# Kernel tuning notes

Measured on AMD Instinct MI355X. Metric: run time of the kernel, lower is better.

## Reference

```python
import jax, jax.numpy as jnp
import numpy as np

B, N, C_IN, C_OUT = 8, 4096, 64, 64
NEG_INF = -9e15
LEAKY_SLOPE = 0.01  # torch F.leaky_relu default


def setup_inputs() -> dict:
    key = jax.random.key(0)
    kx, ka, kw, kq, kk = jax.random.split(key, 5)
    X = jax.random.normal(kx, (B, N, C_IN), dtype=jnp.float32)
    A = jax.random.randint(ka, (N, N), 0, 2, dtype=jnp.int32)
    # xavier_uniform with gain=1.414 ~ scaled uniform; plain scaled normal is fine for a numeric reference
    def xavier(k, shape):
        fan_in, fan_out = shape
        bound = 1.414 * np.sqrt(6.0 / (fan_in + fan_out))
        return jax.random.uniform(k, shape, jnp.float32, -bound, bound)
    weight = xavier(kw, (C_IN, C_OUT))
    query = xavier(kq, (C_IN, C_OUT))
    key_p = xavier(kk, (C_IN, C_OUT))
    return {"X": X, "A": A, "weight": weight, "query": query, "key_p": key_p}


def reference(X, A, weight, query, key_p):
    n = X.shape[1]
    idx = jnp.arange(n)
    adj = A.at[idx, idx].set(1)  # add self-loops
    out = jnp.einsum('bni,io->bno', X, weight)
    q = jnp.einsum('bni,io->bno', X, query)
    k = jnp.einsum('bni,io->bno', X, key_p)
    att = jnp.einsum('bnd,bmd->bnm', q, k)          # QK^T, (B,N,N)
    att = jax.nn.leaky_relu(att, LEAKY_SLOPE)
    att = jnp.where(adj[None, :, :] > 0, att, NEG_INF)
    att = jax.nn.softmax(att, axis=-1)
    # dropout p=0 and/or eval mode -> identity
    return jnp.einsum('bnm,bmo->bno', att, out)
```

## Files before the change

kernel.cpp:

```cpp
#include <hip/hip_runtime.h>
#include <stdint.h>

#define BATCH 8
#define NN 4096
#define CC 64
#define MASKV -1.0e30f
#define LOG2E 1.4426950408889634f

typedef _Float16 half8 __attribute__((ext_vector_type(8)));
typedef __fp16 fp16x2 __attribute__((ext_vector_type(2)));
typedef float f32x4 __attribute__((ext_vector_type(4)));
typedef float f32x16 __attribute__((ext_vector_type(16)));

__device__ __forceinline__ unsigned pk_rtz(float a, float b) {
    union { fp16x2 h; unsigned u; } r;
    r.h = __builtin_amdgcn_cvt_pkrtz(a, b);
    return r.u;
}

__global__ __launch_bounds__(256) void gat_proj(
    const float* __restrict__ X, const float* __restrict__ W0,
    const float* __restrict__ Wq, const float* __restrict__ Wk,
    _Float16* __restrict__ qh,
    _Float16* __restrict__ kb, _Float16* __restrict__ vt)
{
    __shared__ alignas(16) _Float16 WTh[3][64][72];
    __shared__ alignas(16) _Float16 WTl[3][64][72];
    const int t = threadIdx.x;
    const float* Ws[3] = {W0, Wq, Wk};
    for (int e = t; e < 4096; e += 256) {
        int k = e >> 6, c = e & 63;
        #pragma unroll
        for (int m = 0; m < 3; ++m) {
            float w = Ws[m][e];
            _Float16 hi = (_Float16)w;
            WTh[m][c][k] = hi;
            WTl[m][c][k] = (_Float16)(w - (float)hi);
        }
    }
    __syncthreads();
    const int lane = t & 63, wv = t >> 6;
    const int cl = lane & 15, g = lane >> 4;
    {
        int tile = blockIdx.x * 4 + wv;
        int gr = tile * 16;
        const float* xr = X + (size_t)(gr + cl) * CC;
        half8 xh[2], xl[2];
        #pragma unroll
        for (int kf = 0; kf < 2; ++kf) {
            f32x4 a0 = *(const f32x4*)(xr + g*8 + kf*32);
            f32x4 a1 = *(const f32x4*)(xr + g*8 + kf*32 + 4);
            half8 h, l;
            #pragma unroll
            for (int j = 0; j < 4; ++j) {
                _Float16 h0 = (_Float16)a0[j], h1 = (_Float16)a1[j];
                h[j]   = h0; l[j]   = (_Float16)(a0[j] - (float)h0);
                h[j+4] = h1; l[j+4] = (_Float16)(a1[j] - (float)h1);
            }
            xh[kf] = h; xl[kf] = l;
        }
        #pragma unroll
        for (int mat = 1; mat <= 2; ++mat) {
            #pragma unroll
            for (int nt = 0; nt < 4; ++nt) {
                f32x4 acc = {0.f, 0.f, 0.f, 0.f};
                #pragma unroll
                for (int kf = 0; kf < 2; ++kf) {
                    half8 bh = *(const half8*)&WTh[mat][nt*16 + cl][g*8 + kf*32];
                    half8 bl = *(const half8*)&WTl[mat][nt*16 + cl][g*8 + kf*32];
                    acc = __builtin_amdgcn_mfma_f32_16x16x32_f16(xh[kf], bh, acc, 0, 0, 0);
                    acc = __builtin_amdgcn_mfma_f32_16x16x32_f16(xl[kf], bh, acc, 0, 0, 0);
                    acc = __builtin_amdgcn_mfma_f32_16x16x32_f16(xh[kf], bl, acc, 0, 0, 0);
                }
                #pragma unroll
                for (int i = 0; i < 4; ++i) {
                    size_t off = (size_t)(gr + 4*g + i) * CC + nt*16 + cl;
                    if (mat == 1) qh[off] = (_Float16)(acc[i] * LOG2E);
                    else          kb[off] = (_Float16)acc[i];
                }
            }
        }
        {
            int b = gr >> 12, n0 = gr & (NN - 1);
            #pragma unroll
            for (int mt = 0; mt < 4; ++mt) {
                f32x4 acc = {0.f, 0.f, 0.f, 0.f};
                #pragma unroll
                for (int kf = 0; kf < 2; ++kf) {
                    half8 ah = *(const half8*)&WTh[0][mt*16 + cl][g*8 + kf*32];
                    half8 al = *(const half8*)&WTl[0][mt*16 + cl][g*8 + kf*32];
                    acc = __builtin_amdgcn_mfma_f32_16x16x32_f16(ah, xh[kf], acc, 0, 0, 0);
                    acc = __builtin_amdgcn_mfma_f32_16x16x32_f16(al, xh[kf], acc, 0, 0, 0);
                    acc = __builtin_amdgcn_mfma_f32_16x16x32_f16(ah, xl[kf], acc, 0, 0, 0);
                }
                #pragma unroll
                for (int i = 0; i < 4; ++i) {
                    int co = mt*16 + 4*g + i;
                    vt[((size_t)b * CC + co) * NN + n0 + cl] = (_Float16)acc[i];
                }
            }
        }
    }
}

__global__ __launch_bounds__(256) void gat_mask(const int* __restrict__ A,
                                                unsigned short* __restrict__ M16)
{
    const int row = blockIdx.x;
    const int w16 = threadIdx.x;
    const int4* ap = (const int4*)(A + (size_t)row * NN + w16 * 16);
    unsigned m = 0;
    #pragma unroll
    for (int j = 0; j < 4; ++j) {
        int4 a = ap[j];
        m |= (a.x != 0 ? 1u : 0u) << (4*j);
        m |= (a.y != 0 ? 1u : 0u) << (4*j + 1);
        m |= (a.z != 0 ? 1u : 0u) << (4*j + 2);
        m |= (a.w != 0 ? 1u : 0u) << (4*j + 3);
    }
    if (w16 == (row >> 4)) m |= 1u << (row & 15);
    M16[(size_t)row * 256 + w16] = (unsigned short)m;
}

__global__ __launch_bounds__(256) void gat_attn(
    const _Float16* __restrict__ qg,
    const _Float16* __restrict__ kf16, const _Float16* __restrict__ vtb,
    const unsigned long long* __restrict__ M,
    _Float16* __restrict__ po, float2* __restrict__ pml)
{
    __shared__ alignas(16) _Float16 Kt[2][64][64];
    __shared__ alignas(16) _Float16 Vt[2][64][64];
    __shared__ alignas(8) uint2 LUT[16];
    const int t = threadIdx.x;
    const int lane = t & 63, wv = t >> 6;
    const int q32 = lane & 31, hi = lane >> 5;
    const int blk = blockIdx.x;
    const int b  = blk & 7;
    const int sp = (blk >> 3) & 3;
    const int qb = blk >> 5;
    const int Q0 = qb * 128 + wv * 32;
    const int c0 = sp * 16;
    const int swz = (q32 & 7) << 4;

    if (t < 16) {
        unsigned n = t;
        LUT[n] = make_uint2(((n & 1u) ? 0x0000FFFFu : 0u) | ((n & 2u) ? 0xFFFF0000u : 0u),
                            ((n & 4u) ? 0x0000FFFFu : 0u) | ((n & 8u) ? 0xFFFF0000u : 0u));
    }

    const int soff = (((t >> 3) * 128 + (t & 7) * 16) ^ (((t >> 3) & 7) << 4));

    half8 qf[4];
    {
        const _Float16* qr = qg + ((size_t)b * NN + Q0 + q32) * CC + hi * 8;
        #pragma unroll
        for (int kf = 0; kf < 4; ++kf) qf[kf] = *(const half8*)(qr + kf * 16);
    }
    const _Float16* kg = kf16 + (size_t)b * NN * CC;
    const _Float16* vg = vtb + (size_t)b * CC * NN;

    f32x16 o0 = {}, o1 = {};
    float m_run = 0.f, l_run = 0.f;

    uint4 pk0, pk1, pv0, pv1;
    unsigned long long pm;
    auto loadchunk = [&](int kcg) {
        const uint4* ks = (const uint4*)(kg + (size_t)kcg * 64 * CC);
        pk0 = ks[t];
        pk1 = ks[t + 256];
        const _Float16* vs = vg + kcg * 64;
        pv0 = *(const uint4*)(vs + (size_t)(t >> 3) * NN + (t & 7) * 8);
        pv1 = *(const uint4*)(vs + (size_t)((t >> 3) + 32) * NN + (t & 7) * 8);
        pm  = M[(size_t)(Q0 + q32) * 64 + kcg];
    };
    auto stash = [&](int bufi) {
        char* kd = (char*)&Kt[bufi][0][0];
        char* vd = (char*)&Vt[bufi][0][0];
        *(uint4*)(kd + soff) = pk0;
        *(uint4*)(kd + soff + 4096) = pk1;
        *(uint4*)(vd + soff) = pv0;
        *(uint4*)(vd + soff + 4096) = pv1;
    };
    auto pkmax = [](unsigned a, unsigned b) {
        unsigned d;
        asm("v_pk_max_f16 %0, %1, %2" : "=v"(d) : "v"(a), "v"(b));
        return d;
    };

    loadchunk(c0);
    unsigned long long cm = pm;
    stash(0);
    __syncthreads();

    for (int kc = 0; kc < 16; ++kc) {
        const int cur = kc & 1;
        if (kc < 15) loadchunk(c0 + kc + 1);

        const char* kbase = (const char*)&Kt[cur][0][0] + q32 * 128;
        __builtin_amdgcn_s_setprio(1);
        f32x16 s0 = {}, s1 = {};
        #pragma unroll
        for (int kf = 0; kf < 4; ++kf) {
            const int col = (kf * 32 + hi * 16) ^ swz;
            half8 ka0 = *(const half8*)(kbase + col);
            half8 ka1 = *(const half8*)(kbase + 4096 + col);
            s0 = __builtin_amdgcn_mfma_f32_32x32x16_f16(ka0, qf[kf], s0, 0, 0, 0);
            s1 = __builtin_amdgcn_mfma_f32_32x32x16_f16(ka1, qf[kf], s1, 0, 0, 0);
        }
        __builtin_amdgcn_s_setprio(0);

        const unsigned wlo = (unsigned)cm, whi = (unsigned)(cm >> 32);
        unsigned hm[16];
        #pragma unroll
        for (int kt = 0; kt < 2; ++kt) {
            unsigned w = kt ? whi : wlo;
            #pragma unroll
            for (int a = 0; a < 4; ++a) {
                unsigned nib = (w >> (8 * a + 4 * hi)) & 15u;
                uint2 e = LUT[nib];
                hm[kt*8 + 2*a]     = e.x;
                hm[kt*8 + 2*a + 1] = e.y;
            }
        }
        {
            unsigned sm[16];
            #pragma unroll
            for (int j = 0; j < 8; ++j) {
                sm[j]   = pk_rtz(s0[2*j], s0[2*j+1]) & hm[j];
                sm[8+j] = pk_rtz(s1[2*j], s1[2*j+1]) & hm[8+j];
            }
            unsigned u0 = pkmax(pkmax(pkmax(sm[0],sm[1]),  pkmax(sm[2],sm[3])),
                                pkmax(pkmax(sm[4],sm[5]),  pkmax(sm[6],sm[7])));
            unsigned u1 = pkmax(pkmax(pkmax(sm[8],sm[9]),  pkmax(sm[10],sm[11])),
                                pkmax(pkmax(sm[12],sm[13]),pkmax(sm[14],sm[15])));
            union { unsigned u; fp16x2 h; } tu; tu.u = pkmax(u0, u1);
            float mx = fmaxf(fmaxf((float)tu.h[0], (float)tu.h[1]), 0.f);
            mx = fmaxf(mx, __shfl_xor(mx, 32));
            if (__any(mx > m_run)) {
                float nm = fmaxf(m_run, mx);
                float alpha = __builtin_amdgcn_exp2f(m_run - nm);
                m_run = nm;
                l_run *= alpha;
                #pragma unroll
                for (int i = 0; i < 16; ++i) { o0[i] *= alpha; o1[i] *= alpha; }
            }
        }
        unsigned wp[16];
        #pragma unroll
        for (int j = 0; j < 8; ++j) {
            float p0 = __builtin_amdgcn_exp2f(fmaxf(s0[2*j]   - m_run, fmaf(0.01f, s0[2*j],   -m_run)));
            float p1 = __builtin_amdgcn_exp2f(fmaxf(s0[2*j+1] - m_run, fmaf(0.01f, s0[2*j+1], -m_run)));
            float p2 = __builtin_amdgcn_exp2f(fmaxf(s1[2*j]   - m_run, fmaf(0.01f, s1[2*j],   -m_run)));
            float p3 = __builtin_amdgcn_exp2f(fmaxf(s1[2*j+1] - m_run, fmaf(0.01f, s1[2*j+1], -m_run)));
            wp[j]   = pk_rtz(p0, p1) & hm[j];
            wp[8+j] = pk_rtz(p2, p3) & hm[8+j];
        }
        {
            union { unsigned u; fp16x2 h; } z; z.u = 0u;
            fp16x2 acc = z.h;
            #pragma unroll
            for (int j4 = 0; j4 < 4; ++j4) {
                union { unsigned u; fp16x2 h; } x0, x1, x2, x3;
                x0.u = wp[4*j4]; x1.u = wp[4*j4+1]; x2.u = wp[4*j4+2]; x3.u = wp[4*j4+3];
                acc += (x0.h + x1.h) + (x2.h + x3.h);
            }
            l_run += (float)acc[0] + (float)acc[1];
        }
        if (kc < 15) stash(cur ^ 1);
        #pragma unroll
        for (int g4 = 0; g4 < 4; ++g4) {
            unsigned w0 = wp[4*g4+0], w1 = wp[4*g4+1];
            unsigned w2 = wp[4*g4+2], w3 = wp[4*g4+3];
            unsigned u = hi ? w0 : w2;
            unsigned v = hi ? w1 : w3;
            unsigned su = (unsigned)__shfl_xor((int)u, 32);
            unsigned sv = (unsigned)__shfl_xor((int)v, 32);
            wp[4*g4+0] = hi ? su : w0;
            wp[4*g4+1] = hi ? sv : w1;
            wp[4*g4+2] = hi ? w2 : su;
            wp[4*g4+3] = hi ? w3 : sv;
        }
        const char* vb = (const char*)&Vt[cur][0][0] + q32 * 128;
        __builtin_amdgcn_s_setprio(1);
        #pragma unroll
        for (int kc4 = 0; kc4 < 4; ++kc4) {
            union { unsigned u[4]; half8 h; } pb;
            pb.u[0] = wp[4*kc4+0]; pb.u[1] = wp[4*kc4+1];
            pb.u[2] = wp[4*kc4+2]; pb.u[3] = wp[4*kc4+3];
            const int col = (kc4 * 32 + hi * 16) ^ swz;
            half8 vf0 = *(const half8*)(vb + col);
            half8 vf1 = *(const half8*)(vb + 4096 + col);
            o0 = __builtin_amdgcn_mfma_f32_32x32x16_f16(vf0, pb.h, o0, 0, 0, 0);
            o1 = __builtin_amdgcn_mfma_f32_32x32x16_f16(vf1, pb.h, o1, 0, 0, 0);
        }
        __builtin_amdgcn_s_setprio(0);
        cm = pm;
        if (kc < 15) __syncthreads();
    }

    float lt = l_run + __shfl_xor(l_run, 32);
    size_t base = (size_t)sp * (BATCH * NN) + (size_t)b * NN + Q0 + q32;
    _Float16* orow = po + base * 64;
    #pragma unroll
    for (int a = 0; a < 4; ++a) {
        {
            uint2 ow = { pk_rtz(o0[4*a], o0[4*a+1]), pk_rtz(o0[4*a+2], o0[4*a+3]) };
            *(uint2*)(orow + 8*a + 4*hi) = ow;
        }
        {
            uint2 ow = { pk_rtz(o1[4*a], o1[4*a+1]), pk_rtz(o1[4*a+2], o1[4*a+3]) };
            *(uint2*)(orow + 32 + 8*a + 4*hi) = ow;
        }
    }
    if (hi == 0) pml[base] = make_float2(m_run, lt);
}

__global__ __launch_bounds__(256) void gat_comb(
    const _Float16* __restrict__ po, const float2* __restrict__ pml,
    float* __restrict__ out)
{
    int gid = blockIdx.x * 256 + threadIdx.x;
    int row = gid >> 2;
    int col = (gid & 3) * 16;
    float2 ml[4];
    float Mx = MASKV;
    #pragma unroll
    for (int s = 0; s < 4; ++s) {
        ml[s] = pml[s * (BATCH * NN) + row];
        Mx = fmaxf(Mx, ml[s].x);
    }
    float w[4], den = 0.f;
    #pragma unroll
    for (int s = 0; s < 4; ++s) {
        w[s] = __builtin_amdgcn_exp2f(ml[s].x - Mx);
        den += w[s] * ml[s].y;
    }
    float inv = 1.0f / den;
    float acc[16] = {};
    #pragma unroll
    for (int s = 0; s < 4; ++s) {
        const _Float16* p = po + ((size_t)s * (BATCH * NN) + row) * 64 + col;
        float a = w[s] * inv;
        half8 v0 = *(const half8*)(p);
        half8 v1 = *(const half8*)(p + 8);
        #pragma unroll
        for (int j = 0; j < 8; ++j) {
            acc[j]     += a * (float)v0[j];
            acc[j + 8] += a * (float)v1[j];
        }
    }
    float* op = out + (size_t)row * 64 + col;
    #pragma unroll
    for (int i = 0; i < 4; ++i) {
        f32x4 r = {acc[4*i], acc[4*i+1], acc[4*i+2], acc[4*i+3]};
        *(f32x4*)(op + i*4) = r;
    }
}

extern "C" void kernel_launch(void* const* d_in, const int* in_sizes, int n_in,
                              void* d_out, int out_size, void* d_ws, size_t ws_size,
                              hipStream_t stream) {
    const float* X  = (const float*)d_in[0];
    const int*   A  = (const int*)d_in[1];
    const float* W0 = (const float*)d_in[2];
    const float* Wq = (const float*)d_in[3];
    const float* Wk = (const float*)d_in[4];
    float* out = (float*)d_out;
    char* ws = (char*)d_ws;
    const size_t SZ = (size_t)BATCH * NN * CC * 2;
    _Float16* qh  = (_Float16*)(ws);
    _Float16* kbf = (_Float16*)(ws + SZ);
    _Float16* vtb = (_Float16*)(ws + 2*SZ);
    char* Mbase = ws + 3*SZ;
    _Float16* po = (_Float16*)(Mbase + 2*1024*1024);
    float2* pml  = (float2*)(Mbase + 2*1024*1024 + 4*SZ);

    hipLaunchKernelGGL(gat_proj, dim3(512),  dim3(256), 0, stream, X, W0, Wq, Wk, qh, kbf, vtb);
    hipLaunchKernelGGL(gat_mask, dim3(4096), dim3(256), 0, stream, A, (unsigned short*)Mbase);
    hipLaunchKernelGGL(gat_attn, dim3(1024), dim3(256), 0, stream, qh, kbf, vtb,
                       (const unsigned long long*)Mbase, po, pml);
    hipLaunchKernelGGL(gat_comb, dim3(512),  dim3(256), 0, stream, po, pml, out);
}
```

Before: 199.2 us.

## Merge projection and mask kernels, stage K/V via direct global-to-LDS loads

Fuses the projection and mask-packing kernels into one launch, using the extra blocks for mask rows. This saves a launch and lets the two kinds of work overlap. The attention kernel stages K and V tiles with global_load_lds, where two waves handle K and two handle V, replacing register loads followed by LDS stores. This removes the staging registers and the separate stash step. It also adds a lazy-rescale threshold so the running max is only updated when it grows by more than 8, and normalizes partial outputs by l before writing them. The combine kernel's weighting is adjusted to match. The lazy max risks fp16 overflow if the threshold is too large.

After: 194.4 us. 2.4% less time.

```diff
diff --git a/kernel.cpp b/kernel.cpp
--- a/kernel.cpp
+++ b/kernel.cpp
@@ -12,21 +12,43 @@
 typedef float f32x4 __attribute__((ext_vector_type(4)));
 typedef float f32x16 __attribute__((ext_vector_type(16)));
 
+typedef __attribute__((address_space(1))) const unsigned int gu32;
+typedef __attribute__((address_space(3))) unsigned int lu32;
+#define GLL16(gp, lp) __builtin_amdgcn_global_load_lds( \
+    (gu32*)(uintptr_t)(gp), (lu32*)(unsigned)(uintptr_t)(lp), 16, 0, 0)
+
 __device__ __forceinline__ unsigned pk_rtz(float a, float b) {
     union { fp16x2 h; unsigned u; } r;
     r.h = __builtin_amdgcn_cvt_pkrtz(a, b);
     return r.u;
 }
 
-__global__ __launch_bounds__(256) void gat_proj(
+__global__ __launch_bounds__(256) void gat_prep(
     const float* __restrict__ X, const float* __restrict__ W0,
     const float* __restrict__ Wq, const float* __restrict__ Wk,
-    _Float16* __restrict__ qh,
-    _Float16* __restrict__ kb, _Float16* __restrict__ vt)
+    const int* __restrict__ A,
+    _Float16* __restrict__ qh, _Float16* __restrict__ kb,
+    _Float16* __restrict__ vt, unsigned short* __restrict__ M16)
 {
     __shared__ alignas(16) _Float16 WTh[3][64][72];
     __shared__ alignas(16) _Float16 WTl[3][64][72];
     const int t = threadIdx.x;
+    if (blockIdx.x >= 512) {
+        const int row = blockIdx.x - 512;
+        const int4* ap = (const int4*)(A + (size_t)row * NN + t * 16);
+        unsigned m = 0;
+        #pragma unroll
+        for (int j = 0; j < 4; ++j) {
+            int4 a = ap[j];
+            m |= (a.x != 0 ? 1u : 0u) << (4*j);
+            m |= (a.y != 0 ? 1u : 0u) << (4*j + 1);
+            m |= (a.z != 0 ? 1u : 0u) << (4*j + 2);
+            m |= (a.w != 0 ? 1u : 0u) << (4*j + 3);
+        }
+        if (t == (row >> 4)) m |= 1u << (row & 15);
+        M16[(size_t)row * 256 + t] = (unsigned short)m;
+        return;
+    }
     const float* Ws[3] = {W0, Wq, Wk};
     for (int e = t; e < 4096; e += 256) {
         int k = e >> 6, c = e & 63;
@@ -41,85 +63,64 @@
     __syncthreads();
     const int lane = t & 63, wv = t >> 6;
     const int cl = lane & 15, g = lane >> 4;
+    int tile = blockIdx.x * 4 + wv;
+    int gr = tile * 16;
+    const float* xr = X + (size_t)(gr + cl) * CC;
+    half8 xh[2], xl[2];
+    #pragma unroll
+    for (int kf = 0; kf < 2; ++kf) {
+        f32x4 a0 = *(const f32x4*)(xr + g*8 + kf*32);
+        f32x4 a1 = *(const f32x4*)(xr + g*8 + kf*32 + 4);
+        half8 h, l;
+        #pragma unroll
+        for (int j = 0; j < 4; ++j) {
+            _Float16 h0 = (_Float16)a0[j], h1 = (_Float16)a1[j];
+            h[j]   = h0; l[j]   = (_Float16)(a0[j] - (float)h0);
+            h[j+4] = h1; l[j+4] = (_Float16)(a1[j] - (float)h1);
+        }
+        xh[kf] = h; xl[kf] = l;
+    }
+    #pragma unroll
+    for (int mat = 1; mat <= 2; ++mat) {
+        #pragma unroll
+        for (int nt = 0; nt < 4; ++nt) {
+            f32x4 acc = {0.f, 0.f, 0.f, 0.f};
+            #pragma unroll
+            for (int kf = 0; kf < 2; ++kf) {
+                half8 bh = *(const half8*)&WTh[mat][nt*16 + cl][g*8 + kf*32];
+                half8 bl = *(const half8*)&WTl[mat][nt*16 + cl][g*8 + kf*32];
+                acc = __builtin_amdgcn_mfma_f32_16x16x32_f16(xh[kf], bh, acc, 0, 0, 0);
+                acc = __builtin_amdgcn_mfma_f32_16x16x32_f16(xl[kf], bh, acc, 0, 0, 0);
+                acc = __builtin_amdgcn_mfma_f32_16x16x32_f16(xh[kf], bl, acc, 0, 0, 0);
+            }
+            #pragma unroll
+            for (int i = 0; i < 4; ++i) {
+                size_t off = (size_t)(gr + 4*g + i) * CC + nt*16 + cl;
+                if (mat == 1) qh[off] = (_Float16)(acc[i] * LOG2E);
+                else          kb[off] = (_Float16)acc[i];
+            }
+        }
+    }
     {
-        int tile = blockIdx.x * 4 + wv;
-        int gr = tile * 16;
-        const float* xr = X + (size_t)(gr + cl) * CC;
-        half8 xh[2], xl[2];
-        #pragma unroll
-        for (int kf = 0; kf < 2; ++kf) {
-            f32x4 a0 = *(const f32x4*)(xr + g*8 + kf*32);
-            f32x4 a1 = *(const f32x4*)(xr + g*8 + kf*32 + 4);
-            half8 h, l;
-            #pragma unroll
-            for (int j = 0; j < 4; ++j) {
-                _Float16 h0 = (_Float16)a0[j], h1 = (_Float16)a1[j];
-                h[j]   = h0; l[j]   = (_Float16)(a0[j] - (float)h0);
-                h[j+4] = h1; l[j+4] = (_Float16)(a1[j] - (float)h1);
-            }
-            xh[kf] = h; xl[kf] = l;
-        }
-        #pragma unroll
-        for (int mat = 1; mat <= 2; ++mat) {
-            #pragma unroll
-            for (int nt = 0; nt < 4; ++nt) {
-                f32x4 acc = {0.f, 0.f, 0.f, 0.f};
-                #pragma unroll
-                for (int kf = 0; kf < 2; ++kf) {
-                    half8 bh = *(const half8*)&WTh[mat][nt*16 + cl][g*8 + kf*32];
-                    half8 bl = *(const half8*)&WTl[mat][nt*16 + cl][g*8 + kf*32];
-                    acc = __builtin_amdgcn_mfma_f32_16x16x32_f16(xh[kf], bh, acc, 0, 0, 0);
-                    acc = __builtin_amdgcn_mfma_f32_16x16x32_f16(xl[kf], bh, acc, 0, 0, 0);
-                    acc = __builtin_amdgcn_mfma_f32_16x16x32_f16(xh[kf], bl, acc, 0, 0, 0);
-                }
-                #pragma unroll
-                for (int i = 0; i < 4; ++i) {
-                    size_t off = (size_t)(gr + 4*g + i) * CC + nt*16 + cl;
-                    if (mat == 1) qh[off] = (_Float16)(acc[i] * LOG2E);
-                    else          kb[off] = (_Float16)acc[i];
-                }
-            }
-        }
-        {
-            int b = gr >> 12, n0 = gr & (NN - 1);
-            #pragma unroll
-            for (int mt = 0; mt < 4; ++mt) {
-                f32x4 acc = {0.f, 0.f, 0.f, 0.f};
-                #pragma unroll
-                for (int kf = 0; kf < 2; ++kf) {
-                    half8 ah = *(const half8*)&WTh[0][mt*16 + cl][g*8 + kf*32];
-                    half8 al = *(const half8*)&WTl[0][mt*16 + cl][g*8 + kf*32];
-                    acc = __builtin_amdgcn_mfma_f32_16x16x32_f16(ah, xh[kf], acc, 0, 0, 0);
-                    acc = __builtin_amdgcn_mfma_f32_16x16x32_f16(al, xh[kf], acc, 0, 0, 0);
-                    acc = __builtin_amdgcn_mfma_f32_16x16x32_f16(ah, xl[kf], acc, 0, 0, 0);
-                }
-                #pragma unroll
-                for (int i = 0; i < 4; ++i) {
-                    int co = mt*16 + 4*g + i;
-                    vt[((size_t)b * CC + co) * NN + n0 + cl] = (_Float16)acc[i];
-                }
-            }
-        }
-    }
-}
-
-__global__ __launch_bounds__(256) void gat_mask(const int* __restrict__ A,
-                                                unsigned short* __restrict__ M16)
-{
-    const int row = blockIdx.x;
-    const int w16 = threadIdx.x;
-    const int4* ap = (const int4*)(A + (size_t)row * NN + w16 * 16);
-    unsigned m = 0;
-    #pragma unroll
-    for (int j = 0; j < 4; ++j) {
-        int4 a = ap[j];
-        m |= (a.x != 0 ? 1u : 0u) << (4*j);
-        m |= (a.y != 0 ? 1u : 0u) << (4*j + 1);
-        m |= (a.z != 0 ? 1u : 0u) << (4*j + 2);
-        m |= (a.w != 0 ? 1u : 0u) << (4*j + 3);
-    }
-    if (w16 == (row >> 4)) m |= 1u << (row & 15);
-    M16[(size_t)row * 256 + w16] = (unsigned short)m;
+        int b = gr >> 12, n0 = gr & (NN - 1);
+        #pragma unroll
+        for (int mt = 0; mt < 4; ++mt) {
+            f32x4 acc = {0.f, 0.f, 0.f, 0.f};
+            #pragma unroll
+            for (int kf = 0; kf < 2; ++kf) {
+                half8 ah = *(const half8*)&WTh[0][mt*16 + cl][g*8 + kf*32];
+                half8 al = *(const half8*)&WTl[0][mt*16 + cl][g*8 + kf*32];
+                acc = __builtin_amdgcn_mfma_f32_16x16x32_f16(ah, xh[kf], acc, 0, 0, 0);
+                acc = __builtin_amdgcn_mfma_f32_16x16x32_f16(al, xh[kf], acc, 0, 0, 0);
+                acc = __builtin_amdgcn_mfma_f32_16x16x32_f16(ah, xl[kf], acc, 0, 0, 0);
+            }
+            #pragma unroll
+            for (int i = 0; i < 4; ++i) {
+                int co = mt*16 + 4*g + i;
+                vt[((size_t)b * CC + co) * NN + n0 + cl] = (_Float16)acc[i];
+            }
+        }
+    }
 }
 
 __global__ __launch_bounds__(256) void gat_attn(
@@ -148,38 +149,25 @@
                             ((n & 4u) ? 0x0000FFFFu : 0u) | ((n & 8u) ? 0xFFFF0000u : 0u));
     }
 
-    const int soff = (((t >> 3) * 128 + (t & 7) * 16) ^ (((t >> 3) & 7) << 4));
-
-    half8 qf[4];
-    {
-        const _Float16* qr = qg + ((size_t)b * NN + Q0 + q32) * CC + hi * 8;
-        #pragma unroll
-        for (int kf = 0; kf < 4; ++kf) qf[kf] = *(const half8*)(qr + kf * 16);
-    }
-    const _Float16* kg = kf16 + (size_t)b * NN * CC;
-    const _Float16* vg = vtb + (size_t)b * CC * NN;
-
-    f32x16 o0 = {}, o1 = {};
-    float m_run = 0.f, l_run = 0.f;
-
-    uint4 pk0, pk1, pv0, pv1;
-    unsigned long long pm;
-    auto loadchunk = [&](int kcg) {
-        const uint4* ks = (const uint4*)(kg + (size_t)kcg * 64 * CC);
-        pk0 = ks[t];
-        pk1 = ks[t + 256];
-        const _Float16* vs = vg + kcg * 64;
-        pv0 = *(const uint4*)(vs + (size_t)(t >> 3) * NN + (t & 7) * 8);
-        pv1 = *(const uint4*)(vs + (size_t)((t >> 3) + 32) * NN + (t & 7) * 8);
-        pm  = M[(size_t)(Q0 + q32) * 64 + kcg];
-    };
-    auto stash = [&](int bufi) {
-        char* kd = (char*)&Kt[bufi][0][0];
-        char* vd = (char*)&Vt[bufi][0][0];
-        *(uint4*)(kd + soff) = pk0;
-        *(uint4*)(kd + soff + 4096) = pk1;
-        *(uint4*)(vd + soff) = pv0;
-        *(uint4*)(vd + soff + 4096) = pv1;
+    const int lrow = lane >> 3;
+    const int lcol = ((lane & 7) * 16) ^ (lrow << 4);
+    const bool isK = (wv < 2);
+    const int seg = isK ? wv : (wv - 2);
+    const char* gsrc0 = isK
+        ? (const char*)(kf16 + (size_t)b * NN * CC)
+            + (size_t)c0 * 8192 + (size_t)seg * 4096 + lrow * 128 + lcol
+        : (const char*)(vtb + (size_t)b * CC * NN)
+            + (size_t)c0 * 128 + ((size_t)(seg * 32 + lrow)) * 8192 + lcol;
+    const int istride = isK ? 1024 : 65536;
+    const int cstride = isK ? 8192 : 128;
+
+    auto stage = [&](int rel, int bufi) {
+        const char* s = gsrc0 + (size_t)rel * cstride;
+        char* d = isK ? ((char*)&Kt[bufi][0][0] + seg * 4096)
+                      : ((char*)&Vt[bufi][0][0] + seg * 4096);
+        #pragma unroll
+        for (int i = 0; i < 4; ++i)
+            GLL16(s + i * istride, d + i * 1024);
     };
     auto pkmax = [](unsigned a, unsigned b) {
         unsigned d;
@@ -187,14 +175,28 @@
         return d;
     };
 
-    loadchunk(c0);
-    unsigned long long cm = pm;
-    stash(0);
+    half8 qf[4];
+    {
+        const _Float16* qr = qg + ((size_t)b * NN + Q0 + q32) * CC + hi * 8;
+        #pragma unroll
+        for (int kf = 0; kf < 4; ++kf) qf[kf] = *(const half8*)(qr + kf * 16);
+    }
+    const unsigned long long* Mrow = M + (size_t)(Q0 + q32) * 64 + c0;
+
+    f32x16 o0 = {}, o1 = {};
+    float m_run = 0.f, l_run = 0.f;
+
+    stage(0, 0);
+    unsigned long long cm = Mrow[0];
     __syncthreads();
 
     for (int kc = 0; kc < 16; ++kc) {
         const int cur = kc & 1;
-        if (kc < 15) loadchunk(c0 + kc + 1);
+        unsigned long long pmn = 0;
+        if (kc < 15) {
+            stage(kc + 1, cur ^ 1);
+            pmn = Mrow[kc + 1];
+        }
 
         const char* kbase = (const char*)&Kt[cur][0][0] + q32 * 128;
         __builtin_amdgcn_s_setprio(1);
@@ -236,7 +238,7 @@
             union { unsigned u; fp16x2 h; } tu; tu.u = pkmax(u0, u1);
             float mx = fmaxf(fmaxf((float)tu.h[0], (float)tu.h[1]), 0.f);
             mx = fmaxf(mx, __shfl_xor(mx, 32));
-            if (__any(mx > m_run)) {
+            if (__any(mx > m_run + 8.0f)) {
                 float nm = fmaxf(m_run, mx);
                 float alpha = __builtin_amdgcn_exp2f(m_run - nm);
                 m_run = nm;
@@ -266,7 +268,6 @@
             }
             l_run += (float)acc[0] + (float)acc[1];
         }
-        if (kc < 15) stash(cur ^ 1);
         #pragma unroll
         for (int g4 = 0; g4 < 4; ++g4) {
             unsigned w0 = wp[4*g4+0], w1 = wp[4*g4+1];
@@ -294,21 +295,24 @@
             o1 = __builtin_amdgcn_mfma_f32_32x32x16_f16(vf1, pb.h, o1, 0, 0, 0);
         }
         __builtin_amdgcn_s_setprio(0);
-        cm = pm;
+        cm = pmn;
         if (kc < 15) __syncthreads();
     }
 
     float lt = l_run + __shfl_xor(l_run, 32);
+    float invl = (lt > 0.f) ? 1.0f / lt : 0.f;
     size_t base = (size_t)sp * (BATCH * NN) + (size_t)b * NN + Q0 + q32;
     _Float16* orow = po + base * 64;
     #pragma unroll
     for (int a = 0; a < 4; ++a) {
         {
-            uint2 ow = { pk_rtz(o0[4*a], o0[4*a+1]), pk_rtz(o0[4*a+2], o0[4*a+3]) };
+            uint2 ow = { pk_rtz(o0[4*a] * invl, o0[4*a+1] * invl),
+                         pk_rtz(o0[4*a+2] * invl, o0[4*a+3] * invl) };
             *(uint2*)(orow + 8*a + 4*hi) = ow;
         }
         {
-            uint2 ow = { pk_rtz(o1[4*a], o1[4*a+1]), pk_rtz(o1[4*a+2], o1[4*a+3]) };
+            uint2 ow = { pk_rtz(o1[4*a] * invl, o1[4*a+1] * invl),
+                         pk_rtz(o1[4*a+2] * invl, o1[4*a+3] * invl) };
             *(uint2*)(orow + 32 + 8*a + 4*hi) = ow;
         }
     }
@@ -332,8 +336,8 @@
     float w[4], den = 0.f;
     #pragma unroll
     for (int s = 0; s < 4; ++s) {
-        w[s] = __builtin_amdgcn_exp2f(ml[s].x - Mx);
-        den += w[s] * ml[s].y;
+        w[s] = __builtin_amdgcn_exp2f(ml[s].x - Mx) * ml[s].y;
+        den += w[s];
     }
     float inv = 1.0f / den;
     float acc[16] = {};
@@ -375,8 +379,8 @@
     _Float16* po = (_Float16*)(Mbase + 2*1024*1024);
     float2* pml  = (float2*)(Mbase + 2*1024*1024 + 4*SZ);
 
-    hipLaunchKernelGGL(gat_proj, dim3(512),  dim3(256), 0, stream, X, W0, Wq, Wk, qh, kbf, vtb);
-    hipLaunchKernelGGL(gat_mask, dim3(4096), dim3(256), 0, stream, A, (unsigned short*)Mbase);
+    hipLaunchKernelGGL(gat_prep, dim3(4608), dim3(256), 0, stream,
+                       X, W0, Wq, Wk, A, qh, kbf, vtb, (unsigned short*)Mbase);
     hipLaunchKernelGGL(gat_attn, dim3(1024), dim3(256), 0, stream, qh, kbf, vtb,
                        (const unsigned long long*)Mbase, po, pml);
     hipLaunchKernelGGL(gat_comb, dim3(512),  dim3(256), 0, stream, po, pml, out);
```
